# Kernel optimization log

Measured on AMD Instinct MI355X. Metric: run time of the kernel, lower is better.

The kernel has to match this reference:

```python
import jax, jax.numpy as jnp
from jax import lax
import numpy as np

B, T, F, H = 4096, 512, 8, 16  # batch, seq, n_features, hidden_dim


def _lstm(x, Wih, Whh, bih, bhh):
    """PyTorch-convention LSTM over batch-first x [B,T,in].
    Returns (h_T [B,H], outputs [B,T,H]). Gate order: i, f, g, o."""
    Bn = x.shape[0]
    Hn = Whh.shape[1]
    xs = jnp.swapaxes(x, 0, 1)                       # [T,B,in]
    x_proj = xs @ Wih.T + (bih + bhh)                # precompute input GEMM: [T,B,4H]

    def step(carry, xp):
        h, c = carry
        gates = xp + h @ Whh.T                       # [B,4H]
        i, f, g, o = jnp.split(gates, 4, axis=-1)
        i = jax.nn.sigmoid(i)
        f = jax.nn.sigmoid(f)
        g = jnp.tanh(g)
        o = jax.nn.sigmoid(o)
        c = f * c + i * g
        h = o * jnp.tanh(c)
        return (h, c), h

    h0 = jnp.zeros((Bn, Hn), x.dtype)
    (hT, _), hs = lax.scan(step, (h0, h0), x_proj)
    return hT, jnp.swapaxes(hs, 0, 1)                # [B,H], [B,T,H]


def setup_inputs() -> dict:
    key = jax.random.key(0)
    ks = jax.random.split(key, 11)
    s_e = 1.0 / np.sqrt(H)
    u = lambda k, shp: jax.random.uniform(k, shp, jnp.float32, -s_e, s_e)
    return {
        "x": jax.random.normal(ks[0], (B, T, F), jnp.float32),
        "enc_Wih": u(ks[1], (4 * H, F)),
        "enc_Whh": u(ks[2], (4 * H, H)),
        "enc_bih": u(ks[3], (4 * H,)),
        "enc_bhh": u(ks[4], (4 * H,)),
        "dec_Wih": u(ks[5], (4 * H, H)),
        "dec_Whh": u(ks[6], (4 * H, H)),
        "dec_bih": u(ks[7], (4 * H,)),
        "dec_bhh": u(ks[8], (4 * H,)),
        "out_W": u(ks[9], (F, H)),
        "out_b": u(ks[10], (F,)),
    }


def reference(x, enc_Wih, enc_Whh, enc_bih, enc_bhh,
              dec_Wih, dec_Whh, dec_bih, dec_bhh, out_W, out_b):
    # encoder: keep only final hidden state h_T
    hT, _ = _lstm(x, enc_Wih, enc_Whh, enc_bih, enc_bhh)   # [B,H]
    # repeat over time: h.squeeze(0).unsqueeze(1).repeat(1,T,1)
    repeated = jnp.broadcast_to(hT[:, None, :], (x.shape[0], x.shape[1], hT.shape[1]))
    _, decoded = _lstm(repeated, dec_Wih, dec_Whh, dec_bih, dec_bhh)  # [B,T,H]
    return decoded @ out_W.T + out_b                       # [B,T,F]
```

## Files before the change

### kernel.cpp

```cpp
#include <hip/hip_runtime.h>

#define B_ 4096
#define T_ 512
#define F_ 8
#define H_ 16

typedef float f32x2 __attribute__((ext_vector_type(2)));

__device__ __forceinline__ f32x2 pkfma(f32x2 a, f32x2 b, f32x2 c) {
    return __builtin_elementwise_fma(a, b, c);
}

#define LOG2E 1.442695041f
#define N2LOG2E (-2.0f * 1.442695041f)

template <int CTRL>
__device__ __forceinline__ float qperm(float v) {
    int i = __builtin_bit_cast(int, v);
    int rr = __builtin_amdgcn_update_dpp(i, i, CTRL, 0xF, 0xF, false);
    return __builtin_bit_cast(float, rr);
}

__global__ __launch_bounds__(256, 4) void lstm_ae_kernel(
    const float* __restrict__ x,
    const float* __restrict__ eWih, const float* __restrict__ eWhh,
    const float* __restrict__ ebih, const float* __restrict__ ebhh,
    const float* __restrict__ dWih, const float* __restrict__ dWhh,
    const float* __restrict__ dbih, const float* __restrict__ dbhh,
    const float* __restrict__ oW,   const float* __restrict__ ob,
    float* __restrict__ out)
{
    const int tid = threadIdx.x;
    const int ch  = tid >> 6;
    const int l   = tid & 63;
    const int g   = l & 3;
    const int j   = l >> 2;
    const int r   = g * 16 + j;
    const int b   = blockIdx.x * 4 + ch;

    __shared__ __align__(16) f32x2 hbuf2[4][8];
    __shared__ __align__(16) f32x2 xsh2[4][128];

    const bool g0 = (g == 0);
    const float ns1 = (g == 2) ? N2LOG2E : -LOG2E;
    const float m1  = (g == 2) ? 2.0f : 1.0f;
    const float c1  = (g == 2) ? -1.0f : 0.0f;
    const f32x2 zero2 = {0.0f, 0.0f};

    f32x2 wh[8], wi[4];
    {
        const f32x2* w2 = (const f32x2*)(eWhh + r * 16);
#pragma unroll
        for (int p = 0; p < 8; ++p) wh[p] = w2[p];
        const f32x2* wi2 = (const f32x2*)(eWih + r * 8);
#pragma unroll
        for (int p = 0; p < 4; ++p) wi[p] = wi2[p];
    }
    const f32x2 bias2 = {ebih[r] + ebhh[r], 0.0f};

    float c = 0.0f;
    f32x2 hb[8];
#pragma unroll
    for (int p = 0; p < 8; ++p) hb[p] = zero2;
    if (l < 8) hbuf2[ch][l] = zero2;
    __builtin_amdgcn_wave_barrier();

    const float* xb = x + (size_t)b * (T_ * F_);
    float4 nx = *(const float4*)(xb + l * 4);

    for (int c0 = 0; c0 < T_; c0 += 32) {
        __builtin_amdgcn_wave_barrier();
        *(float4*)&xsh2[ch][l * 2] = nx;
        __builtin_amdgcn_wave_barrier();
        if (c0 + 32 < T_)
            nx = *(const float4*)(xb + (c0 + 32) * F_ + l * 4);
        for (int s = 0; s < 32; ++s) {
            f32x2 x0 = xsh2[ch][s * 4 + 0];
            f32x2 x1 = xsh2[ch][s * 4 + 1];
            f32x2 x2 = xsh2[ch][s * 4 + 2];
            f32x2 x3 = xsh2[ch][s * 4 + 3];

            f32x2 aa = pkfma(wi[0], x0, bias2);
            f32x2 ab = pkfma(wi[1], x1, zero2);
            aa = pkfma(wi[2], x2, aa);
            ab = pkfma(wi[3], x3, ab);
#pragma unroll
            for (int p = 0; p < 8; p += 2) {
                aa = pkfma(wh[p],   hb[p],   aa);
                ab = pkfma(wh[p+1], hb[p+1], ab);
            }
            f32x2 t = aa + ab;
            const float acc = t.x + t.y;

            const float a = __builtin_fmaf(
                m1, __builtin_amdgcn_rcpf(1.0f + __builtin_amdgcn_exp2f(ns1 * acc)), c1);
            const float e1 = qperm<0xB1>(a);
            const float e2 = qperm<0x4E>(a);
            const float e3 = qperm<0x1B>(a);
            c = __builtin_fmaf(e1, c, a * e2);
            const float rt = __builtin_amdgcn_rcpf(
                1.0f + __builtin_amdgcn_exp2f(N2LOG2E * c));
            const float h = __builtin_fmaf(e3 + e3, rt, -e3);

            __builtin_amdgcn_wave_barrier();
            if (g0) ((float*)&hbuf2[ch][0])[j] = h;
            __builtin_amdgcn_wave_barrier();
#pragma unroll
            for (int p = 0; p < 8; ++p) hb[p] = hbuf2[ch][p];
        }
    }

    f32x2 wd[8], wo2[8];
    f32x2 xp2;
    {
        f32x2 pa = {dbih[r] + dbhh[r], 0.0f};
        f32x2 pb = zero2;
        const f32x2* wih2 = (const f32x2*)(dWih + r * 16);
#pragma unroll
        for (int p = 0; p < 8; p += 2) {
            pa = pkfma(wih2[p],   hb[p],   pa);
            pb = pkfma(wih2[p+1], hb[p+1], pb);
        }
        f32x2 t = pa + pb;
        xp2 = f32x2{t.x + t.y, 0.0f};
        const f32x2* whh2 = (const f32x2*)(dWhh + r * 16);
#pragma unroll
        for (int p = 0; p < 8; ++p) wd[p] = whh2[p];
        const f32x2* wo = (const f32x2*)(oW + (l & 7) * 16);
#pragma unroll
        for (int p = 0; p < 8; ++p) wo2[p] = wo[p];
    }
    const f32x2 ob2 = {ob[l & 7], 0.0f};
    const bool l8 = (l < 8);

    c = 0.0f;
#pragma unroll
    for (int p = 0; p < 8; ++p) hb[p] = zero2;
    __builtin_amdgcn_wave_barrier();

    float* outp = out + (size_t)b * (T_ * F_);

    for (int t = 0; t < T_; ++t) {
        f32x2 aa = pkfma(wd[0], hb[0], xp2);
        f32x2 ab = pkfma(wd[1], hb[1], zero2);
#pragma unroll
        for (int p = 2; p < 8; p += 2) {
            aa = pkfma(wd[p],   hb[p],   aa);
            ab = pkfma(wd[p+1], hb[p+1], ab);
        }
        f32x2 tt = aa + ab;
        const float acc = tt.x + tt.y;

        const float a = __builtin_fmaf(
            m1, __builtin_amdgcn_rcpf(1.0f + __builtin_amdgcn_exp2f(ns1 * acc)), c1);
        const float e1 = qperm<0xB1>(a);
        const float e2 = qperm<0x4E>(a);
        const float e3 = qperm<0x1B>(a);
        c = __builtin_fmaf(e1, c, a * e2);
        const float rt = __builtin_amdgcn_rcpf(
            1.0f + __builtin_amdgcn_exp2f(N2LOG2E * c));
        const float h = __builtin_fmaf(e3 + e3, rt, -e3);

        __builtin_amdgcn_wave_barrier();
        if (g0) ((float*)&hbuf2[ch][0])[j] = h;
        __builtin_amdgcn_wave_barrier();
#pragma unroll
        for (int p = 0; p < 8; ++p) hb[p] = hbuf2[ch][p];

        f32x2 oa = pkfma(wo2[0], hb[0], ob2);
        f32x2 obb = pkfma(wo2[1], hb[1], zero2);
#pragma unroll
        for (int p = 2; p < 8; p += 2) {
            oa  = pkfma(wo2[p],   hb[p],   oa);
            obb = pkfma(wo2[p+1], hb[p+1], obb);
        }
        f32x2 to = oa + obb;
        if (l8) outp[t * F_ + l] = to.x + to.y;
    }
}

extern "C" void kernel_launch(void* const* d_in, const int* in_sizes, int n_in,
                              void* d_out, int out_size, void* d_ws, size_t ws_size,
                              hipStream_t stream) {
    (void)in_sizes; (void)n_in; (void)d_ws; (void)ws_size; (void)out_size;
    lstm_ae_kernel<<<dim3(B_ / 4), dim3(256), 0, stream>>>(
        (const float*)d_in[0],
        (const float*)d_in[1], (const float*)d_in[2],
        (const float*)d_in[3], (const float*)d_in[4],
        (const float*)d_in[5], (const float*)d_in[6],
        (const float*)d_in[7], (const float*)d_in[8],
        (const float*)d_in[9], (const float*)d_in[10],
        (float*)d_out);
}
```

Baseline: 427.8 us.

## Move LSTM recurrences onto MFMA with split fp16 hi/lo operands

Replaces the per-lane fp32 packed-FMA gate dot products with 16x16x16 fp16 MFMA instructions. Four batch rows share each wave, and the recurrent state h is kept as a B-fragment in registers, which removes the LDS round trip and DPP gate exchange on every step. fp32 accuracy is approximated by splitting weights, inputs and h into fp16 hi/lo pairs and running three to five MFMAs per gate block. Occupancy drops to one wave per SIMD, so latency hiding shrinks, and the split fp16 arithmetic carries some precision risk.

Measured after the change: 545.5 us. 27.5% more time.

```diff
diff --git a/kernel.cpp b/kernel.cpp
--- a/kernel.cpp
+++ b/kernel.cpp
@@ -5,23 +5,39 @@
 #define F_ 8
 #define H_ 16
 
-typedef float f32x2 __attribute__((ext_vector_type(2)));
-
-__device__ __forceinline__ f32x2 pkfma(f32x2 a, f32x2 b, f32x2 c) {
-    return __builtin_elementwise_fma(a, b, c);
-}
+typedef __fp16 f16;
+typedef __fp16 f16x2 __attribute__((ext_vector_type(2)));
+typedef __fp16 f16x4 __attribute__((ext_vector_type(4)));
+typedef float f32x4 __attribute__((ext_vector_type(4)));
 
 #define LOG2E 1.442695041f
-#define N2LOG2E (-2.0f * 1.442695041f)
-
-template <int CTRL>
-__device__ __forceinline__ float qperm(float v) {
-    int i = __builtin_bit_cast(int, v);
-    int rr = __builtin_amdgcn_update_dpp(i, i, CTRL, 0xF, 0xF, false);
-    return __builtin_bit_cast(float, rr);
-}
-
-__global__ __launch_bounds__(256, 4) void lstm_ae_kernel(
+#define N2LOG2E (-2.885390082f)
+
+__device__ __forceinline__ float sigf(float x) {
+    return __builtin_amdgcn_rcpf(1.0f + __builtin_amdgcn_exp2f(-LOG2E * x));
+}
+__device__ __forceinline__ float tanh_f(float x) {
+    return __builtin_fmaf(2.0f,
+        __builtin_amdgcn_rcpf(1.0f + __builtin_amdgcn_exp2f(N2LOG2E * x)), -1.0f);
+}
+
+__device__ __forceinline__ f16x4 mk4(f16x2 a, f16x2 b) {
+    f16x4 r; r[0] = a[0]; r[1] = a[1]; r[2] = b[0]; r[3] = b[1]; return r;
+}
+
+__device__ __forceinline__ f32x4 mfma16(f16x4 a, f16x4 b, f32x4 c) {
+    return __builtin_amdgcn_mfma_f32_16x16x16f16(a, b, c, 0, 0, 0);
+}
+
+__device__ __forceinline__ void split_hl(f32x4 w, f16x4& hi, f16x4& lo) {
+    f16x2 h0 = __builtin_amdgcn_cvt_pkrtz(w[0], w[1]);
+    f16x2 h1 = __builtin_amdgcn_cvt_pkrtz(w[2], w[3]);
+    f16x2 l0 = __builtin_amdgcn_cvt_pkrtz(w[0] - (float)h0[0], w[1] - (float)h0[1]);
+    f16x2 l1 = __builtin_amdgcn_cvt_pkrtz(w[2] - (float)h1[0], w[3] - (float)h1[1]);
+    hi = mk4(h0, h1); lo = mk4(l0, l1);
+}
+
+__global__ __launch_bounds__(256, 1) void lstm_ae_kernel(
     const float* __restrict__ x,
     const float* __restrict__ eWih, const float* __restrict__ eWhh,
     const float* __restrict__ ebih, const float* __restrict__ ebhh,
@@ -30,152 +46,161 @@
     const float* __restrict__ oW,   const float* __restrict__ ob,
     float* __restrict__ out)
 {
-    const int tid = threadIdx.x;
-    const int ch  = tid >> 6;
-    const int l   = tid & 63;
-    const int g   = l & 3;
-    const int j   = l >> 2;
-    const int r   = g * 16 + j;
-    const int b   = blockIdx.x * 4 + ch;
-
-    __shared__ __align__(16) f32x2 hbuf2[4][8];
-    __shared__ __align__(16) f32x2 xsh2[4][128];
-
-    const bool g0 = (g == 0);
-    const float ns1 = (g == 2) ? N2LOG2E : -LOG2E;
-    const float m1  = (g == 2) ? 2.0f : 1.0f;
-    const float c1  = (g == 2) ? -1.0f : 0.0f;
-    const f32x2 zero2 = {0.0f, 0.0f};
-
-    f32x2 wh[8], wi[4];
+    const int l  = threadIdx.x & 63;
+    const int wv = threadIdx.x >> 6;
+    const int n  = l & 15;
+    const int q  = l >> 4;
+    const int b0 = (blockIdx.x * 4 + wv) * 4;
+    const bool ldx = (n < 4);
+    const f16x4 zf = {};
+
+    f16x4 ehh_hi[4], ehh_lo[4], eih[4], eih_hi[4];
+    f32x4 biasE[4];
+#pragma unroll
+    for (int blk = 0; blk < 4; ++blk) {
+        const int m = blk * 16 + n;
+        f32x4 w = *(const f32x4*)(eWhh + m * 16 + 4 * q);
+        split_hl(w, ehh_hi[blk], ehh_lo[blk]);
+        f32x4 wx = *(const f32x4*)(eWih + m * 8 + (q & 1) * 4);
+        f16x4 xh, xl; split_hl(wx, xh, xl);
+        eih[blk]    = (q < 2) ? xh : xl;
+        eih_hi[blk] = (q < 2) ? xh : zf;
+        f32x4 b1 = *(const f32x4*)(ebih + blk * 16 + 4 * q);
+        f32x4 b2 = *(const f32x4*)(ebhh + blk * 16 + 4 * q);
+        biasE[blk] = b1 + b2;
+    }
+
+    float cst[4] = {0.0f, 0.0f, 0.0f, 0.0f};
+    f16x4 Bh_hi = zf, Bh_lo = zf;
+
+    const float* xb = x + (size_t)(b0 + n) * (T_ * F_) + (q & 1) * 4;
+    f32x4 xr[4] = {};
+    if (ldx) {
+        xr[0] = *(const f32x4*)(xb + 0 * F_);
+        xr[1] = *(const f32x4*)(xb + 1 * F_);
+        xr[2] = *(const f32x4*)(xb + 2 * F_);
+    }
+
+    for (int t = 0; t < T_; t += 4) {
+#pragma unroll
+        for (int u = 0; u < 4; ++u) {
+            const int tt = t + u;
+            f32x4 xv = xr[u];
+            if (ldx && tt + 3 < T_)
+                xr[(u + 3) & 3] = *(const f32x4*)(xb + (tt + 3) * F_);
+            f16x2 xh0 = __builtin_amdgcn_cvt_pkrtz(xv[0], xv[1]);
+            f16x2 xh1 = __builtin_amdgcn_cvt_pkrtz(xv[2], xv[3]);
+            f16x4 Bx = mk4(xh0, xh1);
+            f16x2 xl0 = __builtin_amdgcn_cvt_pkrtz(xv[0] - (float)xh0[0],
+                                                   xv[1] - (float)xh0[1]);
+            f16x2 xl1 = __builtin_amdgcn_cvt_pkrtz(xv[2] - (float)xh1[0],
+                                                   xv[3] - (float)xh1[1]);
+            f16x4 Bxl = mk4(xl0, xl1);
+
+            f32x4 acc[4];
+#pragma unroll
+            for (int blk = 0; blk < 4; ++blk)
+                acc[blk] = mfma16(eih[blk], Bx, biasE[blk]);
+#pragma unroll
+            for (int blk = 0; blk < 4; ++blk)
+                acc[blk] = mfma16(eih_hi[blk], Bxl, acc[blk]);
+#pragma unroll
+            for (int blk = 0; blk < 4; ++blk)
+                acc[blk] = mfma16(ehh_hi[blk], Bh_hi, acc[blk]);
+#pragma unroll
+            for (int blk = 0; blk < 4; ++blk)
+                acc[blk] = mfma16(ehh_lo[blk], Bh_hi, acc[blk]);
+#pragma unroll
+            for (int blk = 0; blk < 4; ++blk)
+                acc[blk] = mfma16(ehh_hi[blk], Bh_lo, acc[blk]);
+
+            float hv[4];
+#pragma unroll
+            for (int e = 0; e < 4; ++e) {
+                float gi = sigf(acc[0][e]);
+                float gf = sigf(acc[1][e]);
+                float gg = tanh_f(acc[2][e]);
+                float go = sigf(acc[3][e]);
+                cst[e] = __builtin_fmaf(gf, cst[e], gi * gg);
+                hv[e]  = go * tanh_f(cst[e]);
+            }
+            f16x2 p0 = __builtin_amdgcn_cvt_pkrtz(hv[0], hv[1]);
+            f16x2 p1 = __builtin_amdgcn_cvt_pkrtz(hv[2], hv[3]);
+            Bh_hi = mk4(p0, p1);
+            f16x2 r0 = __builtin_amdgcn_cvt_pkrtz(hv[0] - (float)p0[0],
+                                                  hv[1] - (float)p0[1]);
+            f16x2 r1 = __builtin_amdgcn_cvt_pkrtz(hv[2] - (float)p1[0],
+                                                  hv[3] - (float)p1[1]);
+            Bh_lo = mk4(r0, r1);
+        }
+    }
+
+    f16x4 dhh_hi[4], dhh_lo[4], oWhi, oWlo;
+    f32x4 xpC[4], obC = {};
+#pragma unroll
+    for (int blk = 0; blk < 4; ++blk) {
+        const int m = blk * 16 + n;
+        f32x4 w = *(const f32x4*)(dWhh + m * 16 + 4 * q);
+        split_hl(w, dhh_hi[blk], dhh_lo[blk]);
+        f32x4 wi = *(const f32x4*)(dWih + m * 16 + 4 * q);
+        f16x4 dih_hi, dih_lo; split_hl(wi, dih_hi, dih_lo);
+        f32x4 bb = *(const f32x4*)(dbih + blk * 16 + 4 * q);
+        f32x4 b2 = *(const f32x4*)(dbhh + blk * 16 + 4 * q);
+        bb = bb + b2;
+        f32x4 p = mfma16(dih_hi, Bh_hi, bb);
+        p = mfma16(dih_lo, Bh_hi, p);
+        p = mfma16(dih_hi, Bh_lo, p);
+        xpC[blk] = p;
+    }
     {
-        const f32x2* w2 = (const f32x2*)(eWhh + r * 16);
-#pragma unroll
-        for (int p = 0; p < 8; ++p) wh[p] = w2[p];
-        const f32x2* wi2 = (const f32x2*)(eWih + r * 8);
-#pragma unroll
-        for (int p = 0; p < 4; ++p) wi[p] = wi2[p];
-    }
-    const f32x2 bias2 = {ebih[r] + ebhh[r], 0.0f};
-
-    float c = 0.0f;
-    f32x2 hb[8];
-#pragma unroll
-    for (int p = 0; p < 8; ++p) hb[p] = zero2;
-    if (l < 8) hbuf2[ch][l] = zero2;
-    __builtin_amdgcn_wave_barrier();
-
-    const float* xb = x + (size_t)b * (T_ * F_);
-    float4 nx = *(const float4*)(xb + l * 4);
-
-    for (int c0 = 0; c0 < T_; c0 += 32) {
-        __builtin_amdgcn_wave_barrier();
-        *(float4*)&xsh2[ch][l * 2] = nx;
-        __builtin_amdgcn_wave_barrier();
-        if (c0 + 32 < T_)
-            nx = *(const float4*)(xb + (c0 + 32) * F_ + l * 4);
-        for (int s = 0; s < 32; ++s) {
-            f32x2 x0 = xsh2[ch][s * 4 + 0];
-            f32x2 x1 = xsh2[ch][s * 4 + 1];
-            f32x2 x2 = xsh2[ch][s * 4 + 2];
-            f32x2 x3 = xsh2[ch][s * 4 + 3];
-
-            f32x2 aa = pkfma(wi[0], x0, bias2);
-            f32x2 ab = pkfma(wi[1], x1, zero2);
-            aa = pkfma(wi[2], x2, aa);
-            ab = pkfma(wi[3], x3, ab);
-#pragma unroll
-            for (int p = 0; p < 8; p += 2) {
-                aa = pkfma(wh[p],   hb[p],   aa);
-                ab = pkfma(wh[p+1], hb[p+1], ab);
-            }
-            f32x2 t = aa + ab;
-            const float acc = t.x + t.y;
-
-            const float a = __builtin_fmaf(
-                m1, __builtin_amdgcn_rcpf(1.0f + __builtin_amdgcn_exp2f(ns1 * acc)), c1);
-            const float e1 = qperm<0xB1>(a);
-            const float e2 = qperm<0x4E>(a);
-            const float e3 = qperm<0x1B>(a);
-            c = __builtin_fmaf(e1, c, a * e2);
-            const float rt = __builtin_amdgcn_rcpf(
-                1.0f + __builtin_amdgcn_exp2f(N2LOG2E * c));
-            const float h = __builtin_fmaf(e3 + e3, rt, -e3);
-
-            __builtin_amdgcn_wave_barrier();
-            if (g0) ((float*)&hbuf2[ch][0])[j] = h;
-            __builtin_amdgcn_wave_barrier();
-#pragma unroll
-            for (int p = 0; p < 8; ++p) hb[p] = hbuf2[ch][p];
+        f32x4 wo = {};
+        if (n < 8) wo = *(const f32x4*)(oW + n * 16 + 4 * q);
+        split_hl(wo, oWhi, oWlo);
+        if (q < 2) obC = *(const f32x4*)(ob + 4 * q);
+    }
+
+    cst[0] = cst[1] = cst[2] = cst[3] = 0.0f;
+    Bh_hi = zf; Bh_lo = zf;
+
+    const size_t obase = (size_t)(b0 + n) * (T_ * F_) + 4 * q;
+    const bool stv = (n < 4) && (q < 2);
+
+#pragma unroll 2
+    for (int t = 0; t < T_; ++t) {
+        f32x4 acc[4];
+#pragma unroll
+        for (int blk = 0; blk < 4; ++blk)
+            acc[blk] = mfma16(dhh_hi[blk], Bh_hi, xpC[blk]);
+#pragma unroll
+        for (int blk = 0; blk < 4; ++blk)
+            acc[blk] = mfma16(dhh_lo[blk], Bh_hi, acc[blk]);
+#pragma unroll
+        for (int blk = 0; blk < 4; ++blk)
+            acc[blk] = mfma16(dhh_hi[blk], Bh_lo, acc[blk]);
+
+        float hv[4];
+#pragma unroll
+        for (int e = 0; e < 4; ++e) {
+            float gi = sigf(acc[0][e]);
+            float gf = sigf(acc[1][e]);
+            float gg = tanh_f(acc[2][e]);
+            float go = sigf(acc[3][e]);
+            cst[e] = __builtin_fmaf(gf, cst[e], gi * gg);
+            hv[e]  = go * tanh_f(cst[e]);
         }
-    }
-
-    f32x2 wd[8], wo2[8];
-    f32x2 xp2;
-    {
-        f32x2 pa = {dbih[r] + dbhh[r], 0.0f};
-        f32x2 pb = zero2;
-        const f32x2* wih2 = (const f32x2*)(dWih + r * 16);
-#pragma unroll
-        for (int p = 0; p < 8; p += 2) {
-            pa = pkfma(wih2[p],   hb[p],   pa);
-            pb = pkfma(wih2[p+1], hb[p+1], pb);
-        }
-        f32x2 t = pa + pb;
-        xp2 = f32x2{t.x + t.y, 0.0f};
-        const f32x2* whh2 = (const f32x2*)(dWhh + r * 16);
-#pragma unroll
-        for (int p = 0; p < 8; ++p) wd[p] = whh2[p];
-        const f32x2* wo = (const f32x2*)(oW + (l & 7) * 16);
-#pragma unroll
-        for (int p = 0; p < 8; ++p) wo2[p] = wo[p];
-    }
-    const f32x2 ob2 = {ob[l & 7], 0.0f};
-    const bool l8 = (l < 8);
-
-    c = 0.0f;
-#pragma unroll
-    for (int p = 0; p < 8; ++p) hb[p] = zero2;
-    __builtin_amdgcn_wave_barrier();
-
-    float* outp = out + (size_t)b * (T_ * F_);
-
-    for (int t = 0; t < T_; ++t) {
-        f32x2 aa = pkfma(wd[0], hb[0], xp2);
-        f32x2 ab = pkfma(wd[1], hb[1], zero2);
-#pragma unroll
-        for (int p = 2; p < 8; p += 2) {
-            aa = pkfma(wd[p],   hb[p],   aa);
-            ab = pkfma(wd[p+1], hb[p+1], ab);
-        }
-        f32x2 tt = aa + ab;
-        const float acc = tt.x + tt.y;
-
-        const float a = __builtin_fmaf(
-            m1, __builtin_amdgcn_rcpf(1.0f + __builtin_amdgcn_exp2f(ns1 * acc)), c1);
-        const float e1 = qperm<0xB1>(a);
-        const float e2 = qperm<0x4E>(a);
-        const float e3 = qperm<0x1B>(a);
-        c = __builtin_fmaf(e1, c, a * e2);
-        const float rt = __builtin_amdgcn_rcpf(
-            1.0f + __builtin_amdgcn_exp2f(N2LOG2E * c));
-        const float h = __builtin_fmaf(e3 + e3, rt, -e3);
-
-        __builtin_amdgcn_wave_barrier();
-        if (g0) ((float*)&hbuf2[ch][0])[j] = h;
-        __builtin_amdgcn_wave_barrier();
-#pragma unroll
-        for (int p = 0; p < 8; ++p) hb[p] = hbuf2[ch][p];
-
-        f32x2 oa = pkfma(wo2[0], hb[0], ob2);
-        f32x2 obb = pkfma(wo2[1], hb[1], zero2);
-#pragma unroll
-        for (int p = 2; p < 8; p += 2) {
-            oa  = pkfma(wo2[p],   hb[p],   oa);
-            obb = pkfma(wo2[p+1], hb[p+1], obb);
-        }
-        f32x2 to = oa + obb;
-        if (l8) outp[t * F_ + l] = to.x + to.y;
+        f16x2 p0 = __builtin_amdgcn_cvt_pkrtz(hv[0], hv[1]);
+        f16x2 p1 = __builtin_amdgcn_cvt_pkrtz(hv[2], hv[3]);
+        Bh_hi = mk4(p0, p1);
+        f16x2 r0 = __builtin_amdgcn_cvt_pkrtz(hv[0] - (float)p0[0],
+                                              hv[1] - (float)p0[1]);
+        f16x2 r1 = __builtin_amdgcn_cvt_pkrtz(hv[2] - (float)p1[0],
+                                              hv[3] - (float)p1[1]);
+        Bh_lo = mk4(r0, r1);
+
+        f32x4 oacc = mfma16(oWhi, Bh_hi, obC);
+        oacc = mfma16(oWlo, Bh_hi, oacc);
+        oacc = mfma16(oWhi, Bh_lo, oacc);
+        if (stv) *(f32x4*)(out + obase + (size_t)t * F_) = oacc;
     }
 }
 
@@ -183,7 +208,7 @@
                               void* d_out, int out_size, void* d_ws, size_t ws_size,
                               hipStream_t stream) {
     (void)in_sizes; (void)n_in; (void)d_ws; (void)ws_size; (void)out_size;
-    lstm_ae_kernel<<<dim3(B_ / 4), dim3(256), 0, stream>>>(
+    lstm_ae_kernel<<<dim3(B_ / 16), dim3(256), 0, stream>>>(
         (const float*)d_in[0],
         (const float*)d_in[1], (const float*)d_in[2],
         (const float*)d_in[3], (const float*)d_in[4],
```

## Map one hidden unit per lane with all four gates, four sequences per wave

Applied to the files above, without the earlier changes.

Changes the work split so each lane computes all four gates for one hidden unit, letting a wave handle four batch sequences instead of one. This removes the cross-lane DPP gate exchange and cuts the number of waves and steps per sequence, at the cost of four times the FMAs per lane and more registers for weights. The x staging, the LDS hidden-state layout with vector reads, and the launch bounds and grid size are adjusted to fit the new mapping.

Result: faster. 353.9 us (-17.3%).

```diff
diff --git a/kernel.cpp b/kernel.cpp
--- a/kernel.cpp
+++ b/kernel.cpp
@@ -6,22 +6,25 @@
 #define H_ 16
 
 typedef float f32x2 __attribute__((ext_vector_type(2)));
+typedef float f32x4v __attribute__((ext_vector_type(4)));
 
 __device__ __forceinline__ f32x2 pkfma(f32x2 a, f32x2 b, f32x2 c) {
     return __builtin_elementwise_fma(a, b, c);
 }
+#define SV2(v, a, b) __builtin_shufflevector(v, v, a, b)
 
 #define LOG2E 1.442695041f
-#define N2LOG2E (-2.0f * 1.442695041f)
-
-template <int CTRL>
-__device__ __forceinline__ float qperm(float v) {
-    int i = __builtin_bit_cast(int, v);
-    int rr = __builtin_amdgcn_update_dpp(i, i, CTRL, 0xF, 0xF, false);
-    return __builtin_bit_cast(float, rr);
-}
-
-__global__ __launch_bounds__(256, 4) void lstm_ae_kernel(
+#define N2LOG2E (-2.885390082f)
+
+__device__ __forceinline__ float sigf(float x) {
+    return __builtin_amdgcn_rcpf(1.0f + __builtin_amdgcn_exp2f(-LOG2E * x));
+}
+__device__ __forceinline__ float tanh_f(float x) {
+    return __builtin_fmaf(2.0f,
+        __builtin_amdgcn_rcpf(1.0f + __builtin_amdgcn_exp2f(N2LOG2E * x)), -1.0f);
+}
+
+__global__ __launch_bounds__(256, 1) void lstm_ae_kernel(
     const float* __restrict__ x,
     const float* __restrict__ eWih, const float* __restrict__ eWhh,
     const float* __restrict__ ebih, const float* __restrict__ ebhh,
@@ -31,151 +34,155 @@
     float* __restrict__ out)
 {
     const int tid = threadIdx.x;
-    const int ch  = tid >> 6;
+    const int wv  = tid >> 6;
     const int l   = tid & 63;
-    const int g   = l & 3;
-    const int j   = l >> 2;
-    const int r   = g * 16 + j;
-    const int b   = blockIdx.x * 4 + ch;
-
-    __shared__ __align__(16) f32x2 hbuf2[4][8];
-    __shared__ __align__(16) f32x2 xsh2[4][128];
-
-    const bool g0 = (g == 0);
-    const float ns1 = (g == 2) ? N2LOG2E : -LOG2E;
-    const float m1  = (g == 2) ? 2.0f : 1.0f;
-    const float c1  = (g == 2) ? -1.0f : 0.0f;
+    const int cw  = l >> 4;
+    const int u   = l & 15;
+    const int bw  = blockIdx.x * 16 + wv * 4;
+    const int b   = bw + cw;
+
+    __shared__ __align__(16) f32x2 hsh[4][40];
+    __shared__ __align__(16) f32x2 xsh[4][4][33][4];
+
     const f32x2 zero2 = {0.0f, 0.0f};
 
-    f32x2 wh[8], wi[4];
-    {
-        const f32x2* w2 = (const f32x2*)(eWhh + r * 16);
-#pragma unroll
-        for (int p = 0; p < 8; ++p) wh[p] = w2[p];
-        const f32x2* wi2 = (const f32x2*)(eWih + r * 8);
-#pragma unroll
-        for (int p = 0; p < 4; ++p) wi[p] = wi2[p];
-    }
-    const f32x2 bias2 = {ebih[r] + ebhh[r], 0.0f};
+    f32x2 wh[4][8], wi[4][4];
+    float bias[4];
+#pragma unroll
+    for (int g = 0; g < 4; ++g) {
+        const int r = g * 16 + u;
+        const f32x2* phh = (const f32x2*)(eWhh + r * 16);
+#pragma unroll
+        for (int p = 0; p < 8; ++p) wh[g][p] = phh[p];
+        const f32x2* pih = (const f32x2*)(eWih + r * 8);
+#pragma unroll
+        for (int p = 0; p < 4; ++p) wi[g][p] = pih[p];
+        bias[g] = ebih[r] + ebhh[r];
+    }
 
     float c = 0.0f;
     f32x2 hb[8];
 #pragma unroll
     for (int p = 0; p < 8; ++p) hb[p] = zero2;
-    if (l < 8) hbuf2[ch][l] = zero2;
-    __builtin_amdgcn_wave_barrier();
-
-    const float* xb = x + (size_t)b * (T_ * F_);
-    float4 nx = *(const float4*)(xb + l * 4);
+
+    float* hp = (float*)&hsh[wv][cw * 10];
+
+    const int ps = l >> 1, phx = l & 1;
+    f32x4v xr[4];
+#pragma unroll
+    for (int i = 0; i < 4; ++i)
+        xr[i] = *(const f32x4v*)(x + ((size_t)(bw + i) * T_ + ps) * F_ + phx * 4);
 
     for (int c0 = 0; c0 < T_; c0 += 32) {
         __builtin_amdgcn_wave_barrier();
-        *(float4*)&xsh2[ch][l * 2] = nx;
-        __builtin_amdgcn_wave_barrier();
-        if (c0 + 32 < T_)
-            nx = *(const float4*)(xb + (c0 + 32) * F_ + l * 4);
+#pragma unroll
+        for (int i = 0; i < 4; ++i)
+            *(f32x4v*)&xsh[wv][i][ps][phx * 2] = xr[i];
+        __builtin_amdgcn_wave_barrier();
+        if (c0 + 32 < T_) {
+#pragma unroll
+            for (int i = 0; i < 4; ++i)
+                xr[i] = *(const f32x4v*)(
+                    x + ((size_t)(bw + i) * T_ + (c0 + 32 + ps)) * F_ + phx * 4);
+        }
         for (int s = 0; s < 32; ++s) {
-            f32x2 x0 = xsh2[ch][s * 4 + 0];
-            f32x2 x1 = xsh2[ch][s * 4 + 1];
-            f32x2 x2 = xsh2[ch][s * 4 + 2];
-            f32x2 x3 = xsh2[ch][s * 4 + 3];
-
-            f32x2 aa = pkfma(wi[0], x0, bias2);
-            f32x2 ab = pkfma(wi[1], x1, zero2);
-            aa = pkfma(wi[2], x2, aa);
-            ab = pkfma(wi[3], x3, ab);
-#pragma unroll
-            for (int p = 0; p < 8; p += 2) {
-                aa = pkfma(wh[p],   hb[p],   aa);
-                ab = pkfma(wh[p+1], hb[p+1], ab);
+            f32x4v xq0 = *(const f32x4v*)&xsh[wv][cw][s][0];
+            f32x4v xq1 = *(const f32x4v*)&xsh[wv][cw][s][2];
+            f32x2 x0 = SV2(xq0, 0, 1), x1 = SV2(xq0, 2, 3);
+            f32x2 x2 = SV2(xq1, 0, 1), x3 = SV2(xq1, 2, 3);
+
+            f32x2 acc[4];
+#pragma unroll
+            for (int g = 0; g < 4; ++g) {
+                f32x2 a = pkfma(wi[g][0], x0, f32x2{bias[g], 0.0f});
+                a = pkfma(wi[g][1], x1, a);
+                a = pkfma(wi[g][2], x2, a);
+                a = pkfma(wi[g][3], x3, a);
+#pragma unroll
+                for (int p = 0; p < 8; ++p) a = pkfma(wh[g][p], hb[p], a);
+                acc[g] = a;
             }
-            f32x2 t = aa + ab;
-            const float acc = t.x + t.y;
-
-            const float a = __builtin_fmaf(
-                m1, __builtin_amdgcn_rcpf(1.0f + __builtin_amdgcn_exp2f(ns1 * acc)), c1);
-            const float e1 = qperm<0xB1>(a);
-            const float e2 = qperm<0x4E>(a);
-            const float e3 = qperm<0x1B>(a);
-            c = __builtin_fmaf(e1, c, a * e2);
-            const float rt = __builtin_amdgcn_rcpf(
-                1.0f + __builtin_amdgcn_exp2f(N2LOG2E * c));
-            const float h = __builtin_fmaf(e3 + e3, rt, -e3);
+            const float gi = sigf(acc[0].x + acc[0].y);
+            const float gf = sigf(acc[1].x + acc[1].y);
+            const float gg = tanh_f(acc[2].x + acc[2].y);
+            const float go = sigf(acc[3].x + acc[3].y);
+            c = __builtin_fmaf(gf, c, gi * gg);
+            const float ht = go * tanh_f(c);
 
             __builtin_amdgcn_wave_barrier();
-            if (g0) ((float*)&hbuf2[ch][0])[j] = h;
+            hp[u] = ht;
             __builtin_amdgcn_wave_barrier();
-#pragma unroll
-            for (int p = 0; p < 8; ++p) hb[p] = hbuf2[ch][p];
+            f32x4v h0 = *(const f32x4v*)&hp[0];
+            f32x4v h1 = *(const f32x4v*)&hp[4];
+            f32x4v h2 = *(const f32x4v*)&hp[8];
+            f32x4v h3 = *(const f32x4v*)&hp[12];
+            hb[0] = SV2(h0, 0, 1); hb[1] = SV2(h0, 2, 3);
+            hb[2] = SV2(h1, 0, 1); hb[3] = SV2(h1, 2, 3);
+            hb[4] = SV2(h2, 0, 1); hb[5] = SV2(h2, 2, 3);
+            hb[6] = SV2(h3, 0, 1); hb[7] = SV2(h3, 2, 3);
         }
     }
 
-    f32x2 wd[8], wo2[8];
-    f32x2 xp2;
+    f32x2 wd[4][8];
+    float xp[4];
+#pragma unroll
+    for (int g = 0; g < 4; ++g) {
+        const int r = g * 16 + u;
+        const f32x2* pih = (const f32x2*)(dWih + r * 16);
+        f32x2 a = zero2;
+#pragma unroll
+        for (int p = 0; p < 8; ++p) a = pkfma(pih[p], hb[p], a);
+        xp[g] = dbih[r] + dbhh[r] + a.x + a.y;
+        const f32x2* phh = (const f32x2*)(dWhh + r * 16);
+#pragma unroll
+        for (int p = 0; p < 8; ++p) wd[g][p] = phh[p];
+    }
+    f32x2 wo[8];
     {
-        f32x2 pa = {dbih[r] + dbhh[r], 0.0f};
-        f32x2 pb = zero2;
-        const f32x2* wih2 = (const f32x2*)(dWih + r * 16);
-#pragma unroll
-        for (int p = 0; p < 8; p += 2) {
-            pa = pkfma(wih2[p],   hb[p],   pa);
-            pb = pkfma(wih2[p+1], hb[p+1], pb);
+        const f32x2* po = (const f32x2*)(oW + (u & 7) * 16);
+#pragma unroll
+        for (int p = 0; p < 8; ++p) wo[p] = po[p];
+    }
+    const float obv = ob[u & 7];
+    const bool st = (u < 8);
+    float* outp = out + (size_t)b * (T_ * F_);
+
+    c = 0.0f;
+#pragma unroll
+    for (int p = 0; p < 8; ++p) hb[p] = zero2;
+
+    for (int t = 0; t < T_; ++t) {
+        f32x2 acc[4];
+#pragma unroll
+        for (int g = 0; g < 4; ++g) {
+            f32x2 a = pkfma(wd[g][0], hb[0], f32x2{xp[g], 0.0f});
+#pragma unroll
+            for (int p = 1; p < 8; ++p) a = pkfma(wd[g][p], hb[p], a);
+            acc[g] = a;
         }
-        f32x2 t = pa + pb;
-        xp2 = f32x2{t.x + t.y, 0.0f};
-        const f32x2* whh2 = (const f32x2*)(dWhh + r * 16);
-#pragma unroll
-        for (int p = 0; p < 8; ++p) wd[p] = whh2[p];
-        const f32x2* wo = (const f32x2*)(oW + (l & 7) * 16);
-#pragma unroll
-        for (int p = 0; p < 8; ++p) wo2[p] = wo[p];
-    }
-    const f32x2 ob2 = {ob[l & 7], 0.0f};
-    const bool l8 = (l < 8);
-
-    c = 0.0f;
-#pragma unroll
-    for (int p = 0; p < 8; ++p) hb[p] = zero2;
-    __builtin_amdgcn_wave_barrier();
-
-    float* outp = out + (size_t)b * (T_ * F_);
-
-    for (int t = 0; t < T_; ++t) {
-        f32x2 aa = pkfma(wd[0], hb[0], xp2);
-        f32x2 ab = pkfma(wd[1], hb[1], zero2);
-#pragma unroll
-        for (int p = 2; p < 8; p += 2) {
-            aa = pkfma(wd[p],   hb[p],   aa);
-            ab = pkfma(wd[p+1], hb[p+1], ab);
-        }
-        f32x2 tt = aa + ab;
-        const float acc = tt.x + tt.y;
-
-        const float a = __builtin_fmaf(
-            m1, __builtin_amdgcn_rcpf(1.0f + __builtin_amdgcn_exp2f(ns1 * acc)), c1);
-        const float e1 = qperm<0xB1>(a);
-        const float e2 = qperm<0x4E>(a);
-        const float e3 = qperm<0x1B>(a);
-        c = __builtin_fmaf(e1, c, a * e2);
-        const float rt = __builtin_amdgcn_rcpf(
-            1.0f + __builtin_amdgcn_exp2f(N2LOG2E * c));
-        const float h = __builtin_fmaf(e3 + e3, rt, -e3);
-
-        __builtin_amdgcn_wave_barrier();
-        if (g0) ((float*)&hbuf2[ch][0])[j] = h;
-        __builtin_amdgcn_wave_barrier();
-#pragma unroll
-        for (int p = 0; p < 8; ++p) hb[p] = hbuf2[ch][p];
-
-        f32x2 oa = pkfma(wo2[0], hb[0], ob2);
-        f32x2 obb = pkfma(wo2[1], hb[1], zero2);
-#pragma unroll
-        for (int p = 2; p < 8; p += 2) {
-            oa  = pkfma(wo2[p],   hb[p],   oa);
-            obb = pkfma(wo2[p+1], hb[p+1], obb);
-        }
-        f32x2 to = oa + obb;
-        if (l8) outp[t * F_ + l] = to.x + to.y;
+        const float gi = sigf(acc[0].x + acc[0].y);
+        const float gf = sigf(acc[1].x + acc[1].y);
+        const float gg = tanh_f(acc[2].x + acc[2].y);
+        const float go = sigf(acc[3].x + acc[3].y);
+        c = __builtin_fmaf(gf, c, gi * gg);
+        const float ht = go * tanh_f(c);
+
+        __builtin_amdgcn_wave_barrier();
+        hp[u] = ht;
+        __builtin_amdgcn_wave_barrier();
+        f32x4v h0 = *(const f32x4v*)&hp[0];
+        f32x4v h1 = *(const f32x4v*)&hp[4];
+        f32x4v h2 = *(const f32x4v*)&hp[8];
+        f32x4v h3 = *(const f32x4v*)&hp[12];
+        hb[0] = SV2(h0, 0, 1); hb[1] = SV2(h0, 2, 3);
+        hb[2] = SV2(h1, 0, 1); hb[3] = SV2(h1, 2, 3);
+        hb[4] = SV2(h2, 0, 1); hb[5] = SV2(h2, 2, 3);
+        hb[6] = SV2(h3, 0, 1); hb[7] = SV2(h3, 2, 3);
+
+        f32x2 oa = pkfma(wo[0], hb[0], f32x2{obv, 0.0f});
+#pragma unroll
+        for (int p = 1; p < 8; ++p) oa = pkfma(wo[p], hb[p], oa);
+        if (st) outp[t * F_ + u] = oa.x + oa.y;
     }
 }
 
@@ -183,7 +190,7 @@
                               void* d_out, int out_size, void* d_ws, size_t ws_size,
                               hipStream_t stream) {
     (void)in_sizes; (void)n_in; (void)d_ws; (void)ws_size; (void)out_size;
-    lstm_ae_kernel<<<dim3(B_ / 4), dim3(256), 0, stream>>>(
+    lstm_ae_kernel<<<dim3(B_ / 16), dim3(256), 0, stream>>>(
         (const float*)d_in[0],
         (const float*)d_in[1], (const float*)d_in[2],
         (const float*)d_in[3], (const float*)d_in[4],
```
